# Kernel optimization log

Measured on AMD Instinct MI355X. Metric: run time of the kernel, lower is better.

The kernel has to match this reference:

```python
import jax, jax.numpy as jnp
import numpy as np

ND, NT, B = 16384, 16384, 4096
FD, FT, C = 256, 256, 768


def _gat(x_src, x_dst, ei, Ws, Wd, a_s, a_d, b, num_dst, self_loops):
    """PyG GATConv, heads=1: per-edge attention softmax over incoming edges."""
    if self_loops:
        loops = jnp.arange(num_dst, dtype=ei.dtype)
        ei = jnp.concatenate([ei, jnp.stack([loops, loops])], axis=1)
    src, dst = ei[0], ei[1]
    hs = x_src @ Ws                                   # [Ns, C]
    hd = x_dst @ Wd                                   # [Ndst, C]
    e = jax.nn.leaky_relu((hs @ a_s)[src] + (hd @ a_d)[dst], 0.2)   # [E]
    m = jax.ops.segment_max(e, dst, num_segments=num_dst)
    p = jnp.exp(e - m[dst])
    s = jax.ops.segment_sum(p, dst, num_segments=num_dst)
    alpha = p / (s[dst] + 1e-16)
    out = jax.ops.segment_sum(hs[src] * alpha[:, None], dst, num_segments=num_dst)
    return out + b


def _l2norm(x):
    n = jnp.linalg.norm(x, axis=1, keepdims=True)
    return x / jnp.maximum(n, 1e-12)


def setup_inputs() -> dict:
    ks = iter(jax.random.split(jax.random.key(0), 64))
    def nrm(shape, fan_in=None):
        s = 1.0 if fan_in is None else (1.0 / fan_in) ** 0.5
        return jax.random.normal(next(ks), shape, jnp.float32) * s
    inp = {}
    inp["x_drug"] = nrm((ND, FD))
    inp["x_target"] = nrm((NT, FT))
    inp["cell_features"] = nrm((B, 890))
    for et, fs, fd in (("dd", FD, FD), ("dt", FD, FT), ("tt", FT, FT)):
        inp[f"W_src_{et}"] = nrm((fs, C), fs)
        inp[f"W_dst_{et}"] = nrm((fd, C), fd)
        inp[f"a_src_{et}"] = nrm((C,), C)
        inp[f"a_dst_{et}"] = nrm((C,), C)
        inp[f"b_{et}"] = jnp.zeros((C,), jnp.float32)
    for name, fi, fo in (("red1", 890, 2048), ("red2", 2048, 512), ("red3", 512, 2 * C),
                         ("r2a", 4 * C, 2048), ("r2b", 2048, 512), ("r2c", 512, C), ("cls", C, 2)):
        inp[f"{name}_w"] = nrm((fi, fo), fi)
        inp[f"{name}_b"] = jnp.zeros((fo,), jnp.float32)
    inp["drug1_id"] = jax.random.randint(next(ks), (B,), 0, ND)
    inp["drug2_id"] = jax.random.randint(next(ks), (B,), 0, ND)
    inp["ei_dd"] = jax.random.randint(next(ks), (2, 131072), 0, ND)
    inp["ei_dt"] = jnp.stack([jax.random.randint(next(ks), (262144,), 0, ND),
                              jax.random.randint(next(ks), (262144,), 0, NT)])
    inp["ei_tt"] = jax.random.randint(next(ks), (2, 262144), 0, NT)
    return inp


def reference(x_drug, x_target, cell_features,
              W_src_dd, W_dst_dd, a_src_dd, a_dst_dd, b_dd,
              W_src_dt, W_dst_dt, a_src_dt, a_dst_dt, b_dt,
              W_src_tt, W_dst_tt, a_src_tt, a_dst_tt, b_tt,
              red1_w, red1_b, red2_w, red2_b, red3_w, red3_b,
              r2a_w, r2a_b, r2b_w, r2b_b, r2c_w, r2c_b,
              cls_w, cls_b,
              drug1_id, drug2_id, ei_dd, ei_dt, ei_tt):
    # HeteroConv (aggr='sum') followed by per-type ReLU, num_layers=1
    drug = jax.nn.relu(_gat(x_drug, x_drug, ei_dd,
                            W_src_dd, W_dst_dd, a_src_dd, a_dst_dd, b_dd, ND, True))
    target = jax.nn.relu(
        _gat(x_drug, x_target, ei_dt, W_src_dt, W_dst_dt, a_src_dt, a_dst_dt, b_dt, NT, False)
        + _gat(x_target, x_target, ei_tt, W_src_tt, W_dst_tt, a_src_tt, a_dst_tt, b_tt, NT, True))
    del target  # with num_layers=1 the target embeddings never feed the output (faithful)
    d1 = drug[drug1_id]
    d2 = drug[drug2_id]
    cell = _l2norm(cell_features)
    cell = jax.nn.relu(cell @ red1_w + red1_b)
    cell = jax.nn.relu(cell @ red2_w + red2_b)
    cell = jax.nn.relu(cell @ red3_w + red3_b)          # [B, 2*C]
    hidden = _l2norm(jnp.concatenate([d1, d2, cell], axis=1))  # [B, 4*C]
    hidden = jax.nn.relu(hidden @ r2a_w + r2a_b)
    hidden = jax.nn.relu(hidden @ r2b_w + r2b_b)
    hidden = jax.nn.relu(hidden @ r2c_w + r2c_b)
    return hidden @ cls_w + cls_b                       # [B, 2]
```

## Files before the change

### kernel.cpp

```cpp
#include <hip/hip_runtime.h>
#include <cstdint>

#define ND 16384
#define BATCH 4096
#define CDIM 768
#define E_DD 131072
#define FD 256

typedef unsigned short u16;
typedef u16 u16x4 __attribute__((ext_vector_type(4)));
typedef u16 u16x8 __attribute__((ext_vector_type(8)));
typedef short s16x8 __attribute__((ext_vector_type(8)));
typedef float f32x4 __attribute__((ext_vector_type(4)));

__device__ __forceinline__ u16 f2bf(float x) {
  union { float f; uint32_t u; } v; v.f = x;
  uint32_t r = v.u + 0x7fffu + ((v.u >> 16) & 1u);
  return (u16)(r >> 16);
}
__device__ __forceinline__ float bf2f(u16 h) {
  union { float f; uint32_t u; } v; v.u = ((uint32_t)h) << 16;
  return v.f;
}
__device__ __forceinline__ uint32_t split2p(float x) {
  u16 h = f2bf(x);
  u16 l = f2bf(x - bf2f(h));
  return ((uint32_t)h << 16) | l;
}

#define GLOAD_LDS16(gp, lp)                                                   \
  __builtin_amdgcn_global_load_lds(                                           \
      (__attribute__((address_space(1))) void*)(gp),                          \
      (__attribute__((address_space(3))) void*)(lp), 16, 0, 0)

#define KP 40

template <int KS, int OUT_BF16, int RELU, int BIAS, int ASPLIT, int ALO, int BLO,
          int BKD, int NW>
__device__ __forceinline__ void gemm_core(
    int bx, int by, int bz,
    const float* __restrict__ Af,
    const u16* __restrict__ Ahi, const u16* __restrict__ Alo,
    const u16* __restrict__ Bhi, const u16* __restrict__ Blo,
    const float* __restrict__ bias,
    float* __restrict__ Cf, u16* __restrict__ Chi,
    int M, int N, int K, u16* AsB, u16* BsB) {
  constexpr int NTH = NW * 64;
  constexpr int WC = (NW == 8) ? 4 : 2;
  constexpr int MT = 4;
  constexpr int NT = (NW == 8) ? 2 : 4;
  constexpr int BM = 128, BN = 128;
  constexpr int ASEG = BM / 64;
  constexpr int BSEG = BN / 64;
  constexpr bool DIRECT = (ASPLIT == 0 && ALO == 0 && BLO == 0);

  const int t = threadIdx.x;
  const int bm0 = bx * BM, bn0 = by * BN;
  const int wid = t >> 6, lane = t & 63;
  const int quad = lane >> 4, l16 = lane & 15;
  const int wm0 = (wid / WC) * (MT * 16);
  const int wn0 = (wid % WC) * (NT * 16);

  const int chunk = K / KS;
  const int kbeg = (KS > 1) ? bz * chunk : 0;
  const int kend = kbeg + chunk;

  float bvv[NT];
#pragma unroll
  for (int ni = 0; ni < NT; ++ni)
    bvv[ni] = BIAS ? bias[bn0 + wn0 + ni * 16 + l16] : 0.f;

  f32x4 acc[MT][NT];
#pragma unroll
  for (int i = 0; i < MT; ++i)
#pragma unroll
    for (int j = 0; j < NT; ++j) acc[i][j] = (f32x4){0.f, 0.f, 0.f, 0.f};

  if constexpr (DIRECT) {
    constexpr int SLOTS = BKD / 8;
    constexpr int SM = SLOTS - 1;
    constexpr int NLD = (BM * BKD) / (NTH * 8);
    auto stageA = [&](int buf, int kk) {
#pragma unroll
      for (int c = 0; c < NLD; ++c) {
        int s = t + NTH * c;
        int r = s / SLOTS, j = s % SLOTS;
        int jj = j ^ (r & SM);
        size_t goff = (size_t)(bm0 + r) * K + kk + jj * 8;
        int lofs = __builtin_amdgcn_readfirstlane((wid * 64 + NTH * c) * 8);
        GLOAD_LDS16(Ahi + goff, AsB + buf * (BM * BKD) + lofs);
      }
    };
    auto stageB = [&](int buf, int kk) {
#pragma unroll
      for (int c = 0; c < NLD; ++c) {
        int s = t + NTH * c;
        int r = s / SLOTS, j = s % SLOTS;
        int jj = j ^ (r & SM);
        size_t goff = (size_t)(bn0 + r) * K + kk + jj * 8;
        int lofs = __builtin_amdgcn_readfirstlane((wid * 64 + NTH * c) * 8);
        GLOAD_LDS16(Bhi + goff, BsB + buf * (BN * BKD) + lofs);
      }
    };
    const int rsw = l16 & SM;
    stageA(0, kbeg);
    stageB(0, kbeg);
    int cur = 0;
    for (int k0 = kbeg;;) {
      __syncthreads();
      int kn = k0 + BKD;
      if (kn < kend) {
        stageA(cur ^ 1, kn);
        stageB(cur ^ 1, kn);
      }
      const u16* Ab = AsB + cur * (BM * BKD);
      const u16* Bb = BsB + cur * (BN * BKD);
#pragma unroll
      for (int h = 0; h < BKD / 32; ++h) {
        s16x8 ah[MT], bh[NT];
#pragma unroll
        for (int mi = 0; mi < MT; ++mi)
          ah[mi] = *(const s16x8*)(Ab + (wm0 + mi * 16 + l16) * BKD +
                                   (((h * 4 + quad) ^ rsw) * 8));
#pragma unroll
        for (int ni = 0; ni < NT; ++ni)
          bh[ni] = *(const s16x8*)(Bb + (wn0 + ni * 16 + l16) * BKD +
                                   (((h * 4 + quad) ^ rsw) * 8));
#pragma unroll
        for (int mi = 0; mi < MT; ++mi)
#pragma unroll
          for (int ni = 0; ni < NT; ++ni)
            acc[mi][ni] = __builtin_amdgcn_mfma_f32_16x16x32_bf16(
                ah[mi], bh[ni], acc[mi][ni], 0, 0, 0);
      }
      k0 = kn;
      cur ^= 1;
      if (k0 >= kend) break;
    }
  } else {
    auto As = [&](int a, int r, int k) -> u16& { return AsB[(a * BM + r) * KP + k]; };
    auto Bs = [&](int a, int r, int k) -> u16& { return BsB[(a * BN + r) * KP + k]; };

    u16x8 pAh[ASEG], pAl[ASEG], pBh[BSEG], pBl[BSEG];

    auto loadA = [&](int c, int kk) {
      int s = t + 256 * c, row = s >> 2, kq = (s & 3) * 8;
      size_t off = (size_t)(bm0 + row) * K + kk + kq;
      if (ASPLIT) {
        f32x4 v0 = *(const f32x4*)(Af + off);
        f32x4 v1 = *(const f32x4*)(Af + off + 4);
        u16x8 h, l;
#pragma unroll
        for (int e = 0; e < 4; ++e) {
          uint32_t p = split2p(v0[e]);
          h[e] = (u16)(p >> 16); l[e] = (u16)(p & 0xffffu);
          uint32_t q = split2p(v1[e]);
          h[e + 4] = (u16)(q >> 16); l[e + 4] = (u16)(q & 0xffffu);
        }
        pAh[c] = h; pAl[c] = l;
      } else {
        pAh[c] = *(const u16x8*)(Ahi + off);
        if (ALO) pAl[c] = *(const u16x8*)(Alo + off);
      }
    };
    auto loadB = [&](int c, int kk) {
      int s = t + 256 * c, row = s >> 2, kq = (s & 3) * 8;
      size_t off = (size_t)(bn0 + row) * K + kk + kq;
      pBh[c] = *(const u16x8*)(Bhi + off);
      if (BLO) pBl[c] = *(const u16x8*)(Blo + off);
    };

#pragma unroll
    for (int c = 0; c < ASEG; ++c) loadA(c, kbeg);
#pragma unroll
    for (int c = 0; c < BSEG; ++c) loadB(c, kbeg);

    for (int k0 = kbeg;;) {
      __syncthreads();
#pragma unroll
      for (int c = 0; c < ASEG; ++c) {
        int s = t + 256 * c, row = s >> 2, kq = (s & 3) * 8;
        *(u16x8*)&As(0, row, kq) = pAh[c];
        if (ALO) *(u16x8*)&As(1, row, kq) = pAl[c];
      }
#pragma unroll
      for (int c = 0; c < BSEG; ++c) {
        int s = t + 256 * c, row = s >> 2, kq = (s & 3) * 8;
        *(u16x8*)&Bs(0, row, kq) = pBh[c];
        if (BLO) *(u16x8*)&Bs(1, row, kq) = pBl[c];
      }
      __syncthreads();

      int kn = k0 + 32;
      if (kn < kend) {
#pragma unroll
        for (int c = 0; c < ASEG; ++c) loadA(c, kn);
#pragma unroll
        for (int c = 0; c < BSEG; ++c) loadB(c, kn);
      }

      s16x8 ah[MT], al[MT], bh[NT], bl[NT];
#pragma unroll
      for (int mi = 0; mi < MT; ++mi) {
        ah[mi] = *(const s16x8*)&As(0, wm0 + mi * 16 + l16, quad * 8);
        if (ALO) al[mi] = *(const s16x8*)&As(1, wm0 + mi * 16 + l16, quad * 8);
      }
#pragma unroll
      for (int ni = 0; ni < NT; ++ni) {
        bh[ni] = *(const s16x8*)&Bs(0, wn0 + ni * 16 + l16, quad * 8);
        if (BLO) bl[ni] = *(const s16x8*)&Bs(1, wn0 + ni * 16 + l16, quad * 8);
      }
#pragma unroll
      for (int mi = 0; mi < MT; ++mi)
#pragma unroll
        for (int ni = 0; ni < NT; ++ni) {
          acc[mi][ni] = __builtin_amdgcn_mfma_f32_16x16x32_bf16(
              ah[mi], bh[ni], acc[mi][ni], 0, 0, 0);
          if (BLO)
            acc[mi][ni] = __builtin_amdgcn_mfma_f32_16x16x32_bf16(
                ah[mi], bl[ni], acc[mi][ni], 0, 0, 0);
          if (ALO)
            acc[mi][ni] = __builtin_amdgcn_mfma_f32_16x16x32_bf16(
                al[mi], bh[ni], acc[mi][ni], 0, 0, 0);
        }
      k0 = kn;
      if (k0 >= kend) break;
    }
  }

  float* Cp = (KS > 1) ? Cf + (size_t)bz * M * N : Cf;
#pragma unroll
  for (int mi = 0; mi < MT; ++mi) {
#pragma unroll
    for (int ni = 0; ni < NT; ++ni) {
      int row = bm0 + wm0 + mi * 16 + quad * 4;
      int col = bn0 + wn0 + ni * 16 + l16;
#pragma unroll
      for (int r = 0; r < 4; ++r) {
        float v = acc[mi][ni][r] + bvv[ni];
        if (RELU) v = fmaxf(v, 0.f);
        size_t o = (size_t)(row + r) * N + col;
        if (OUT_BF16) Chi[o] = f2bf(v);
        else Cp[o] = v;
      }
    }
  }
}

template <int KS, int OUT_BF16, int RELU, int BIAS, int ASPLIT, int ALO, int BLO,
          int BKD, int NW>
__global__ __launch_bounds__(NW * 64) void mfma_gemm(
    const float* __restrict__ Af,
    const u16* __restrict__ Ahi, const u16* __restrict__ Alo,
    const u16* __restrict__ Bhi, const u16* __restrict__ Blo,
    const float* __restrict__ bias,
    float* __restrict__ Cf, u16* __restrict__ Chi,
    int M, int N, int K) {
  constexpr bool DIRECT = (ASPLIT == 0 && ALO == 0 && BLO == 0);
  __shared__ __align__(16) u16 AsB[DIRECT ? 2 * 128 * BKD : (ALO ? 2 : 1) * 128 * KP];
  __shared__ __align__(16) u16 BsB[DIRECT ? 2 * 128 * BKD : (BLO ? 2 : 1) * 128 * KP];
  gemm_core<KS, OUT_BF16, RELU, BIAS, ASPLIT, ALO, BLO, BKD, NW>(
      blockIdx.x, blockIdx.y, (KS > 1) ? (int)blockIdx.z : 0,
      Af, Ahi, Alo, Bhi, Blo, bias, Cf, Chi, M, N, K, AsB, BsB);
}

__device__ __forceinline__ void gat_body(
    int idx, int t,
    const u16* __restrict__ hs, const float* __restrict__ es,
    const float* __restrict__ ed, const int* __restrict__ offsets,
    const int* __restrict__ slots, const float* __restrict__ bias,
    const int* __restrict__ list, const int* __restrict__ cnt,
    u16* __restrict__ out) {
  if (idx >= *cnt) return;
  int d = list[idx];
  int lane = t & 63;
  int beg = offsets[d], end = offsets[d + 1];
  float edv = ed[d];
  float mx = -1e30f;
  for (int j = beg + lane; j < end; j += 64) {
    float e = es[slots[j]] + edv;
    e = e >= 0.f ? e : 0.2f * e;
    mx = fmaxf(mx, e);
  }
#pragma unroll
  for (int m = 32; m; m >>= 1) mx = fmaxf(mx, __shfl_xor(mx, m));
  float sm = 0.f;
  for (int j = beg + lane; j < end; j += 64) {
    float e = es[slots[j]] + edv;
    e = e >= 0.f ? e : 0.2f * e;
    sm += expf(e - mx);
  }
#pragma unroll
  for (int m = 32; m; m >>= 1) sm += __shfl_xor(sm, m);
  float inv = 1.f / (sm + 1e-16f);
  int c8 = lane * 8;
  int c4 = 512 + lane * 4;
  float a8[8] = {};
  float a4[4] = {};
  for (int j = beg; j < end; ++j) {
    int srcn = slots[j];
    float e = es[srcn] + edv;
    e = e >= 0.f ? e : 0.2f * e;
    float alpha = expf(e - mx) * inv;
    const u16* hrow = hs + (size_t)srcn * CDIM;
    u16x8 r8 = *(const u16x8*)(hrow + c8);
    u16x4 r4 = *(const u16x4*)(hrow + c4);
#pragma unroll
    for (int e2 = 0; e2 < 8; ++e2) a8[e2] = fmaf(alpha, bf2f(r8[e2]), a8[e2]);
#pragma unroll
    for (int e2 = 0; e2 < 4; ++e2) a4[e2] = fmaf(alpha, bf2f(r4[e2]), a4[e2]);
  }
  u16* orow = out + (size_t)d * CDIM;
  u16x8 o8;
  u16x4 o4;
#pragma unroll
  for (int e2 = 0; e2 < 8; ++e2) o8[e2] = f2bf(fmaxf(a8[e2] + bias[c8 + e2], 0.f));
#pragma unroll
  for (int e2 = 0; e2 < 4; ++e2) o4[e2] = f2bf(fmaxf(a4[e2] + bias[c4 + e2], 0.f));
  *(u16x8*)(orow + c8) = o8;
  *(u16x4*)(orow + c4) = o4;
}

__global__ __launch_bounds__(256) void gat_aggregate(
    const u16* __restrict__ hs, const float* __restrict__ es,
    const float* __restrict__ ed, const int* __restrict__ offsets,
    const int* __restrict__ slots, const float* __restrict__ bias,
    const int* __restrict__ list, const int* __restrict__ cnt,
    u16* __restrict__ out) {
  gat_body(blockIdx.x * 4 + (threadIdx.x >> 6), threadIdx.x,
           hs, es, ed, offsets, slots, bias, list, cnt, out);
}

__global__ __launch_bounds__(256) void dual_gemm_red1_hs_scatter(
    const u16* __restrict__ cn, const u16* __restrict__ r1T,
    const float* __restrict__ red1_b, u16* __restrict__ c1,
    const float* __restrict__ xd, const u16* __restrict__ wsrcT,
    u16* __restrict__ hs,
    const int* __restrict__ src, const int* __restrict__ dst,
    int* __restrict__ cursor, int* __restrict__ slots) {
  __shared__ __align__(16) u16 SMEM[16384];
  int b = blockIdx.x;
  if (b < 512) {
    gemm_core<1, 1, 1, 1, 0, 0, 0, 32, 4>(b & 31, b >> 5, 0, nullptr, cn, nullptr,
                                          r1T, nullptr, red1_b, nullptr, c1,
                                          BATCH, 2048, 896, SMEM, SMEM + 2 * 128 * 32);
  } else if (b < 1280) {
    int b2 = b - 512;
    gemm_core<1, 1, 0, 0, 1, 1, 0, 32, 4>(b2 & 127, b2 >> 7, 0, xd, nullptr, nullptr,
                                          wsrcT, nullptr, nullptr, nullptr, hs,
                                          ND, CDIM, FD, SMEM, SMEM + 2 * 128 * KP);
  } else {
    int e = (b - 1280) * 256 + threadIdx.x;
    if (e < E_DD) {
      int pos = atomicAdd(&cursor[dst[e]], 1);
      slots[pos] = src[e];
    }
  }
}

template <int KS>
__global__ void reduce_split_ks(const float* __restrict__ P,
                                const float* __restrict__ bias,
                                u16* __restrict__ Chi, int M, int N) {
  int i = blockIdx.x * 256 + threadIdx.x;
  int total = (M * N) >> 2;
  if (i >= total) return;
  f32x4 s = ((const f32x4*)P)[i];
#pragma unroll
  for (int z = 1; z < KS; ++z) s += ((const f32x4*)P)[(size_t)z * total + i];
  int col = (i * 4) % N;
  f32x4 bv = *(const f32x4*)(bias + col);
  u16x4 h;
#pragma unroll
  for (int e = 0; e < 4; ++e) h[e] = f2bf(fmaxf(s[e] + bv[e], 0.f));
  *(u16x4*)&Chi[i * 4] = h;
}

__global__ void reduce_cls(const float* __restrict__ P,
                           const float* __restrict__ bias,
                           const float* __restrict__ clsw,
                           const float* __restrict__ clsb,
                           float* __restrict__ out) {
  int row = blockIdx.x * 4 + (threadIdx.x >> 6);
  int lane = threadIdx.x & 63;
  const f32x4* p0 = (const f32x4*)(P + (size_t)row * CDIM);
  const f32x4* p1 = (const f32x4*)(P + (size_t)BATCH * CDIM + (size_t)row * CDIM);
  float s0 = 0.f, s1 = 0.f;
#pragma unroll
  for (int i = 0; i < 3; ++i) {
    int c4 = lane + 64 * i;
    f32x4 a = p0[c4] + p1[c4];
    f32x4 bv = *(const f32x4*)(bias + c4 * 4);
#pragma unroll
    for (int e = 0; e < 4; ++e) {
      float h = fmaxf(a[e] + bv[e], 0.f);
      int c = c4 * 4 + e;
      s0 = fmaf(h, clsw[c * 2 + 0], s0);
      s1 = fmaf(h, clsw[c * 2 + 1], s1);
    }
  }
#pragma unroll
  for (int m = 32; m; m >>= 1) {
    s0 += __shfl_xor(s0, m);
    s1 += __shfl_xor(s1, m);
  }
  if (lane == 0) {
    out[row * 2 + 0] = s0 + clsb[0];
    out[row * 2 + 1] = s1 + clsb[1];
  }
}

struct TDesc {
  const float* W;
  u16* Th;
  int K, N, Kpad, start;
};
struct TPack { TDesc d[7]; };

#define P1_T 11328
#define P1_W (P1_T + 256)
#define P1_I (P1_W + 64)
__global__ __launch_bounds__(256) void prep1(
    TPack p,
    const float* __restrict__ Wsrc, const float* __restrict__ Wdst,
    const float* __restrict__ a_s, const float* __restrict__ a_d,
    float* __restrict__ wsv, float* __restrict__ wdv,
    int* __restrict__ counts, int* __restrict__ mask, int* __restrict__ cnt,
    const float* __restrict__ cellf, u16* __restrict__ cn_hi) {
  __shared__ __align__(16) float S[1088];
  int b = blockIdx.x;
  int t = threadIdx.x;
  if (b < P1_T) {
    float (*tile)[33] = (float(*)[33])S;
    int mi = 0;
#pragma unroll
    for (int i = 1; i < 7; ++i)
      if (b >= p.d[i].start) mi = i;
    TDesc dd = p.d[mi];
    int rel = b - dd.start;
    int tilesX = dd.Kpad / 32;
    int k0 = (rel % tilesX) * 32, n0 = (rel / tilesX) * 32;
    int tx = t & 31, ty = t >> 5;
#pragma unroll
    for (int i = 0; i < 4; ++i) {
      int k = k0 + ty + 8 * i, n = n0 + tx;
      tile[ty + 8 * i][tx] = (k < dd.K && n < dd.N) ? dd.W[(size_t)k * dd.N + n] : 0.f;
    }
    __syncthreads();
#pragma unroll
    for (int i = 0; i < 4; ++i) {
      int n = n0 + ty + 8 * i, k = k0 + tx;
      if (n < dd.N) dd.Th[(size_t)n * dd.Kpad + k] = f2bf(tile[tx][ty + 8 * i]);
    }
  } else if (b < P1_W) {
    int k = b - P1_T;
    float* rs = S;
    float* rd = S + 256;
    float s = 0.f, d = 0.f;
    for (int c = t; c < CDIM; c += 256) {
      s += Wsrc[(size_t)k * CDIM + c] * a_s[c];
      d += Wdst[(size_t)k * CDIM + c] * a_d[c];
    }
    rs[t] = s; rd[t] = d;
    __syncthreads();
    for (int st = 128; st; st >>= 1) {
      if (t < st) { rs[t] += rs[t + st]; rd[t] += rd[t + st]; }
      __syncthreads();
    }
    if (t == 0) { wsv[k] = rs[0]; wdv[k] = rd[0]; }
  } else if (b < P1_I) {
    int i = (b - P1_W) * 256 + t;
    if (i < ND) { counts[i] = 1; mask[i] = 0; }
    if (i == 0) *cnt = 0;
  } else {
    int row = b - P1_I;
    float* red = S;
    const float* irow = cellf + (size_t)row * 890;
    float s = 0.f;
    for (int c = t; c < 890; c += 256) { float v = irow[c]; s += v * v; }
    red[t] = s;
    __syncthreads();
    for (int st = 128; st; st >>= 1) {
      if (t < st) red[t] += red[t + st];
      __syncthreads();
    }
    float inv = 1.f / fmaxf(sqrtf(red[0]), 1e-12f);
    for (int c = t; c < 896; c += 256) {
      float v = (c < 890) ? irow[c] * inv : 0.f;
      cn_hi[(size_t)row * 896 + c] = f2bf(v);
    }
  }
}

#define P2_E (ND * FD / 1024)
#define P2_M (P2_E + BATCH / 256)
__global__ __launch_bounds__(256) void prep2(
    const float* __restrict__ x, const float* __restrict__ wsv,
    const float* __restrict__ wdv, float* __restrict__ es, float* __restrict__ ed,
    const int* __restrict__ d1, const int* __restrict__ d2, int* __restrict__ mask,
    const int* __restrict__ dst, int* __restrict__ counts) {
  int b = blockIdx.x, t = threadIdx.x;
  if (b < P2_E) {
    int i = b * 256 + t;
    int lane = t & 63;
    int row = i >> 6;
    int c4 = lane * 4;
    f32x4 v = ((const f32x4*)x)[i];
    f32x4 ws = *(const f32x4*)(wsv + c4);
    f32x4 wd = *(const f32x4*)(wdv + c4);
    float a = v[0] * ws[0] + v[1] * ws[1] + v[2] * ws[2] + v[3] * ws[3];
    float bb = v[0] * wd[0] + v[1] * wd[1] + v[2] * wd[2] + v[3] * wd[3];
#pragma unroll
    for (int m = 32; m; m >>= 1) {
      a += __shfl_xor(a, m);
      bb += __shfl_xor(bb, m);
    }
    if (lane == 0) { es[row] = a; ed[row] = bb; }
  } else if (b < P2_M) {
    int i = (b - P2_E) * 256 + t;
    mask[d1[i]] = 1;
    mask[d2[i]] = 1;
  } else {
    int e = (b - P2_M) * 256 + t;
    atomicAdd(&counts[dst[e]], 1);
  }
}

__global__ __launch_bounds__(512) void prep3(
    const int* __restrict__ mask, int* __restrict__ cnt, int* __restrict__ list,
    const int* __restrict__ counts, int* __restrict__ offsets,
    int* __restrict__ cursor, int* __restrict__ slots) {
  __shared__ int part[512];
  int b = blockIdx.x, t = threadIdx.x;
  if (b < 32) {
    int i = b * 512 + t;
    if (mask[i]) {
      int pos = atomicAdd(cnt, 1);
      list[pos] = i;
    }
  } else {
    int base = t * 32;
    int s = 0;
    for (int i = 0; i < 32; ++i) s += counts[base + i];
    part[t] = s;
    __syncthreads();
    if (t == 0) {
      int run = 0;
      for (int i = 0; i < 512; ++i) { int tmp = part[i]; part[i] = run; run += tmp; }
      offsets[ND] = run;
    }
    __syncthreads();
    int run = part[t];
    for (int i = 0; i < 32; ++i) {
      int d = base + i;
      offsets[d] = run;
      slots[run] = d;
      cursor[d] = run + 1;
      run += counts[d];
    }
  }
}

__global__ __launch_bounds__(256) void hidden_build_bf16(
    const u16* __restrict__ drug, const u16* __restrict__ c3,
    const int* __restrict__ d1, const int* __restrict__ d2,
    u16* __restrict__ hhi) {
  int row = blockIdx.x;
  int t = threadIdx.x;
  const u16* s1 = drug + (size_t)d1[row] * CDIM;
  const u16* s2 = drug + (size_t)d2[row] * CDIM;
  const u16* s3 = c3 + (size_t)row * (2 * CDIM);
  float vals[12];
  float ss = 0.f;
#pragma unroll
  for (int i = 0; i < 12; ++i) {
    int c = t + 256 * i;
    float v;
    if (i < 3)      v = bf2f(s1[c]);
    else if (i < 6) v = bf2f(s2[c - CDIM]);
    else            v = bf2f(s3[c - 2 * CDIM]);
    vals[i] = v;
    ss += v * v;
  }
  __shared__ float red[256];
  red[t] = ss;
  __syncthreads();
  for (int st = 128; st; st >>= 1) {
    if (t < st) red[t] += red[t + st];
    __syncthreads();
  }
  float inv = 1.f / fmaxf(sqrtf(red[0]), 1e-12f);
  u16* hrow_h = hhi + (size_t)row * (4 * CDIM);
#pragma unroll
  for (int i = 0; i < 12; ++i) hrow_h[t + 256 * i] = f2bf(vals[i] * inv);
}

extern "C" void kernel_launch(void* const* d_in, const int* in_sizes, int n_in,
                              void* d_out, int out_size, void* d_ws, size_t ws_size,
                              hipStream_t stream) {
  const float* x_drug   = (const float*)d_in[0];
  const float* cellf    = (const float*)d_in[2];
  const float* W_src_dd = (const float*)d_in[3];
  const float* W_dst_dd = (const float*)d_in[4];
  const float* a_src_dd = (const float*)d_in[5];
  const float* a_dst_dd = (const float*)d_in[6];
  const float* b_dd     = (const float*)d_in[7];
  const float* red1_w = (const float*)d_in[18];
  const float* red1_b = (const float*)d_in[19];
  const float* red2_w = (const float*)d_in[20];
  const float* red2_b = (const float*)d_in[21];
  const float* red3_w = (const float*)d_in[22];
  const float* red3_b = (const float*)d_in[23];
  const float* r2a_w  = (const float*)d_in[24];
  const float* r2a_b  = (const float*)d_in[25];
  const float* r2b_w  = (const float*)d_in[26];
  const float* r2b_b  = (const float*)d_in[27];
  const float* r2c_w  = (const float*)d_in[28];
  const float* r2c_b  = (const float*)d_in[29];
  const float* cls_w  = (const float*)d_in[30];
  const float* cls_b  = (const float*)d_in[31];
  const int* drug1_id = (const int*)d_in[32];
  const int* drug2_id = (const int*)d_in[33];
  const int* ei_dd    = (const int*)d_in[34];
  float* out = (float*)d_out;

  const int* dd_src = ei_dd;
  const int* dd_dst = ei_dd + E_DD;

  char* w = (char*)d_ws;
  size_t off = 0;
  auto alloc = [&](size_t bytes) -> char* {
    char* p = w + off;
    off = (off + bytes + 255) & ~(size_t)255;
    return p;
  };
  u16* hs   = (u16*)alloc((size_t)ND * CDIM * 2);
  u16* drug = (u16*)alloc((size_t)ND * CDIM * 2);
  u16* c3   = (u16*)alloc((size_t)BATCH * 2 * CDIM * 2);
  float* P  = (float*)alloc((size_t)4 * BATCH * 512 * 4);
  u16* hid_hi = hs;
  u16* cn_hi = (u16*)alloc((size_t)BATCH * 896 * 2);
  u16* c1_hi = (u16*)alloc((size_t)BATCH * 2048 * 2);
  u16* c2_hi = (u16*)alloc((size_t)BATCH * 512 * 2);
  u16* wsrcT_hi = (u16*)alloc((size_t)CDIM * FD * 2);
  u16* r1T_hi = (u16*)alloc((size_t)2048 * 896 * 2);
  u16* r2T_hi = (u16*)alloc((size_t)512 * 2048 * 2);
  u16* r3T_hi = (u16*)alloc((size_t)1536 * 512 * 2);
  u16* raT_hi = (u16*)alloc((size_t)2048 * 3072 * 2);
  u16* rbT_hi = (u16*)alloc((size_t)512 * 2048 * 2);
  u16* rcT_hi = (u16*)alloc((size_t)768 * 512 * 2);
  float* es  = (float*)alloc((size_t)ND * 4);
  float* ed  = (float*)alloc((size_t)ND * 4);
  float* wsv = (float*)alloc(FD * 4);
  float* wdv = (float*)alloc(FD * 4);
  int* counts  = (int*)alloc((size_t)ND * 4);
  int* offsets = (int*)alloc((size_t)(ND + 1) * 4);
  int* cursor  = (int*)alloc((size_t)ND * 4);
  int* slots   = (int*)alloc((size_t)(E_DD + ND) * 4);
  int* mask    = (int*)alloc((size_t)ND * 4);
  int* list    = (int*)alloc((size_t)ND * 4);
  int* cnt     = (int*)alloc(256);
  (void)ws_size; (void)n_in; (void)in_sizes; (void)out_size;

  TPack tp;
  tp.d[0] = {W_src_dd, wsrcT_hi, 256, 768, 256, 0};
  tp.d[1] = {red1_w, r1T_hi, 890, 2048, 896, 192};
  tp.d[2] = {red2_w, r2T_hi, 2048, 512, 2048, 1984};
  tp.d[3] = {red3_w, r3T_hi, 512, 1536, 512, 3008};
  tp.d[4] = {r2a_w, raT_hi, 3072, 2048, 3072, 3776};
  tp.d[5] = {r2b_w, rbT_hi, 2048, 512, 2048, 9920};
  tp.d[6] = {r2c_w, rcT_hi, 512, 768, 512, 10944};
  prep1<<<15744, 256, 0, stream>>>(tp, W_src_dd, W_dst_dd, a_src_dd, a_dst_dd,
                                   wsv, wdv, counts, mask, cnt, cellf, cn_hi);

  prep2<<<4624, 256, 0, stream>>>(x_drug, wsv, wdv, es, ed, drug1_id, drug2_id,
                                  mask, dd_dst, counts);

  prep3<<<33, 512, 0, stream>>>(mask, cnt, list, counts, offsets, cursor, slots);

  dual_gemm_red1_hs_scatter<<<1792, 256, 0, stream>>>(
      cn_hi, r1T_hi, red1_b, c1_hi, x_drug, wsrcT_hi, hs,
      dd_src, dd_dst, cursor, slots);

  mfma_gemm<4, 0, 0, 0, 0, 0, 0, 64, 8><<<dim3(BATCH / 128, 512 / 128, 4), 512, 0, stream>>>(
      nullptr, c1_hi, nullptr, r2T_hi, nullptr, nullptr, P, nullptr, BATCH, 512, 2048);
  reduce_split_ks<4><<<BATCH * 512 / 1024, 256, 0, stream>>>(P, red2_b, c2_hi, BATCH, 512);
  mfma_gemm<1, 1, 1, 1, 0, 0, 0, 64, 8><<<dim3(BATCH / 128, 1536 / 128), 512, 0, stream>>>(
      nullptr, c2_hi, nullptr, r3T_hi, nullptr, red3_b, nullptr, c3, BATCH, 1536, 512);

  gat_aggregate<<<ND / 4, 256, 0, stream>>>(hs, es, ed, offsets, slots, b_dd, list, cnt, drug);

  hidden_build_bf16<<<BATCH, 256, 0, stream>>>(drug, c3, drug1_id, drug2_id, hid_hi);

  mfma_gemm<1, 1, 1, 1, 0, 0, 0, 64, 8><<<dim3(BATCH / 128, 2048 / 128), 512, 0, stream>>>(
      nullptr, hid_hi, nullptr, raT_hi, nullptr, r2a_b, nullptr, c1_hi, BATCH, 2048, 3072);
  mfma_gemm<4, 0, 0, 0, 0, 0, 0, 64, 8><<<dim3(BATCH / 128, 512 / 128, 4), 512, 0, stream>>>(
      nullptr, c1_hi, nullptr, rbT_hi, nullptr, nullptr, P, nullptr, BATCH, 512, 2048);
  reduce_split_ks<4><<<BATCH * 512 / 1024, 256, 0, stream>>>(P, r2b_b, c2_hi, BATCH, 512);
  mfma_gemm<2, 0, 0, 0, 0, 0, 0, 64, 8><<<dim3(BATCH / 128, CDIM / 128, 2), 512, 0, stream>>>(
      nullptr, c2_hi, nullptr, rcT_hi, nullptr, nullptr, P, nullptr, BATCH, CDIM, 512);
  reduce_cls<<<BATCH / 4, 256, 0, stream>>>(P, r2c_b, cls_w, cls_b, out);
}
```

Measured before the change: 441.5 us.

## Pre-split x_drug into concatenated hi/lo bf16 and run hs GEMM on direct-LDS path

The hs projection previously split fp32 x_drug into hi/lo bf16 inside the GEMM and used a register-staged path with two MFMAs per tile. Now prep2 writes x_drug as [hi|lo] bf16 along K (512 wide) and the W_src transpose is duplicated along K, so hi*W + lo*W becomes one K=512 GEMM on the async global_load_lds double-buffered path. This removes the slower non-direct GEMM branch entirely. In exchange it adds an extra 16 MB write in prep2 and extra reads in the GEMM.

New measurement: 433.6 us. About the same (-1.8%).

```diff
diff --git a/kernel.cpp b/kernel.cpp
--- a/kernel.cpp
+++ b/kernel.cpp
@@ -22,11 +22,6 @@
   union { float f; uint32_t u; } v; v.u = ((uint32_t)h) << 16;
   return v.f;
 }
-__device__ __forceinline__ uint32_t split2p(float x) {
-  u16 h = f2bf(x);
-  u16 l = f2bf(x - bf2f(h));
-  return ((uint32_t)h << 16) | l;
-}
 
 #define GLOAD_LDS16(gp, lp)                                                   \
   __builtin_amdgcn_global_load_lds(                                           \
@@ -35,13 +30,10 @@
 
 #define KP 40
 
-template <int KS, int OUT_BF16, int RELU, int BIAS, int ASPLIT, int ALO, int BLO,
-          int BKD, int NW>
+template <int KS, int OUT_BF16, int RELU, int BIAS, int BKD, int NW>
 __device__ __forceinline__ void gemm_core(
     int bx, int by, int bz,
-    const float* __restrict__ Af,
-    const u16* __restrict__ Ahi, const u16* __restrict__ Alo,
-    const u16* __restrict__ Bhi, const u16* __restrict__ Blo,
+    const u16* __restrict__ Ahi, const u16* __restrict__ Bhi,
     const float* __restrict__ bias,
     float* __restrict__ Cf, u16* __restrict__ Chi,
     int M, int N, int K, u16* AsB, u16* BsB) {
@@ -50,9 +42,6 @@
   constexpr int MT = 4;
   constexpr int NT = (NW == 8) ? 2 : 4;
   constexpr int BM = 128, BN = 128;
-  constexpr int ASEG = BM / 64;
-  constexpr int BSEG = BN / 64;
-  constexpr bool DIRECT = (ASPLIT == 0 && ALO == 0 && BLO == 0);
 
   const int t = threadIdx.x;
   const int bm0 = bx * BM, bn0 = by * BN;
@@ -76,156 +65,65 @@
 #pragma unroll
     for (int j = 0; j < NT; ++j) acc[i][j] = (f32x4){0.f, 0.f, 0.f, 0.f};
 
-  if constexpr (DIRECT) {
-    constexpr int SLOTS = BKD / 8;
-    constexpr int SM = SLOTS - 1;
-    constexpr int NLD = (BM * BKD) / (NTH * 8);
-    auto stageA = [&](int buf, int kk) {
-#pragma unroll
-      for (int c = 0; c < NLD; ++c) {
-        int s = t + NTH * c;
-        int r = s / SLOTS, j = s % SLOTS;
-        int jj = j ^ (r & SM);
-        size_t goff = (size_t)(bm0 + r) * K + kk + jj * 8;
-        int lofs = __builtin_amdgcn_readfirstlane((wid * 64 + NTH * c) * 8);
-        GLOAD_LDS16(Ahi + goff, AsB + buf * (BM * BKD) + lofs);
-      }
-    };
-    auto stageB = [&](int buf, int kk) {
-#pragma unroll
-      for (int c = 0; c < NLD; ++c) {
-        int s = t + NTH * c;
-        int r = s / SLOTS, j = s % SLOTS;
-        int jj = j ^ (r & SM);
-        size_t goff = (size_t)(bn0 + r) * K + kk + jj * 8;
-        int lofs = __builtin_amdgcn_readfirstlane((wid * 64 + NTH * c) * 8);
-        GLOAD_LDS16(Bhi + goff, BsB + buf * (BN * BKD) + lofs);
-      }
-    };
-    const int rsw = l16 & SM;
-    stageA(0, kbeg);
-    stageB(0, kbeg);
-    int cur = 0;
-    for (int k0 = kbeg;;) {
-      __syncthreads();
-      int kn = k0 + BKD;
-      if (kn < kend) {
-        stageA(cur ^ 1, kn);
-        stageB(cur ^ 1, kn);
-      }
-      const u16* Ab = AsB + cur * (BM * BKD);
-      const u16* Bb = BsB + cur * (BN * BKD);
-#pragma unroll
-      for (int h = 0; h < BKD / 32; ++h) {
-        s16x8 ah[MT], bh[NT];
-#pragma unroll
-        for (int mi = 0; mi < MT; ++mi)
-          ah[mi] = *(const s16x8*)(Ab + (wm0 + mi * 16 + l16) * BKD +
-                                   (((h * 4 + quad) ^ rsw) * 8));
+  constexpr int SLOTS = BKD / 8;
+  constexpr int SM = SLOTS - 1;
+  constexpr int NLD = (BM * BKD) / (NTH * 8);
+  auto stageA = [&](int buf, int kk) {
+#pragma unroll
+    for (int c = 0; c < NLD; ++c) {
+      int s = t + NTH * c;
+      int r = s / SLOTS, j = s % SLOTS;
+      int jj = j ^ (r & SM);
+      size_t goff = (size_t)(bm0 + r) * K + kk + jj * 8;
+      int lofs = __builtin_amdgcn_readfirstlane((wid * 64 + NTH * c) * 8);
+      GLOAD_LDS16(Ahi + goff, AsB + buf * (BM * BKD) + lofs);
+    }
+  };
+  auto stageB = [&](int buf, int kk) {
+#pragma unroll
+    for (int c = 0; c < NLD; ++c) {
+      int s = t + NTH * c;
+      int r = s / SLOTS, j = s % SLOTS;
+      int jj = j ^ (r & SM);
+      size_t goff = (size_t)(bn0 + r) * K + kk + jj * 8;
+      int lofs = __builtin_amdgcn_readfirstlane((wid * 64 + NTH * c) * 8);
+      GLOAD_LDS16(Bhi + goff, BsB + buf * (BN * BKD) + lofs);
+    }
+  };
+  const int rsw = l16 & SM;
+  stageA(0, kbeg);
+  stageB(0, kbeg);
+  int cur = 0;
+  for (int k0 = kbeg;;) {
+    __syncthreads();
+    int kn = k0 + BKD;
+    if (kn < kend) {
+      stageA(cur ^ 1, kn);
+      stageB(cur ^ 1, kn);
+    }
+    const u16* Ab = AsB + cur * (BM * BKD);
+    const u16* Bb = BsB + cur * (BN * BKD);
+#pragma unroll
+    for (int h = 0; h < BKD / 32; ++h) {
+      s16x8 ah[MT], bh[NT];
+#pragma unroll
+      for (int mi = 0; mi < MT; ++mi)
+        ah[mi] = *(const s16x8*)(Ab + (wm0 + mi * 16 + l16) * BKD +
+                                 (((h * 4 + quad) ^ rsw) * 8));
+#pragma unroll
+      for (int ni = 0; ni < NT; ++ni)
+        bh[ni] = *(const s16x8*)(Bb + (wn0 + ni * 16 + l16) * BKD +
+                                 (((h * 4 + quad) ^ rsw) * 8));
+#pragma unroll
+      for (int mi = 0; mi < MT; ++mi)
 #pragma unroll
         for (int ni = 0; ni < NT; ++ni)
-          bh[ni] = *(const s16x8*)(Bb + (wn0 + ni * 16 + l16) * BKD +
-                                   (((h * 4 + quad) ^ rsw) * 8));
-#pragma unroll
-        for (int mi = 0; mi < MT; ++mi)
-#pragma unroll
-          for (int ni = 0; ni < NT; ++ni)
-            acc[mi][ni] = __builtin_amdgcn_mfma_f32_16x16x32_bf16(
-                ah[mi], bh[ni], acc[mi][ni], 0, 0, 0);
-      }
-      k0 = kn;
-      cur ^= 1;
-      if (k0 >= kend) break;
-    }
-  } else {
-    auto As = [&](int a, int r, int k) -> u16& { return AsB[(a * BM + r) * KP + k]; };
-    auto Bs = [&](int a, int r, int k) -> u16& { return BsB[(a * BN + r) * KP + k]; };
-
-    u16x8 pAh[ASEG], pAl[ASEG], pBh[BSEG], pBl[BSEG];
-
-    auto loadA = [&](int c, int kk) {
-      int s = t + 256 * c, row = s >> 2, kq = (s & 3) * 8;
-      size_t off = (size_t)(bm0 + row) * K + kk + kq;
-      if (ASPLIT) {
-        f32x4 v0 = *(const f32x4*)(Af + off);
-        f32x4 v1 = *(const f32x4*)(Af + off + 4);
-        u16x8 h, l;
-#pragma unroll
-        for (int e = 0; e < 4; ++e) {
-          uint32_t p = split2p(v0[e]);
-          h[e] = (u16)(p >> 16); l[e] = (u16)(p & 0xffffu);
-          uint32_t q = split2p(v1[e]);
-          h[e + 4] = (u16)(q >> 16); l[e + 4] = (u16)(q & 0xffffu);
-        }
-        pAh[c] = h; pAl[c] = l;
-      } else {
-        pAh[c] = *(const u16x8*)(Ahi + off);
-        if (ALO) pAl[c] = *(const u16x8*)(Alo + off);
-      }
-    };
-    auto loadB = [&](int c, int kk) {
-      int s = t + 256 * c, row = s >> 2, kq = (s & 3) * 8;
-      size_t off = (size_t)(bn0 + row) * K + kk + kq;
-      pBh[c] = *(const u16x8*)(Bhi + off);
-      if (BLO) pBl[c] = *(const u16x8*)(Blo + off);
-    };
-
-#pragma unroll
-    for (int c = 0; c < ASEG; ++c) loadA(c, kbeg);
-#pragma unroll
-    for (int c = 0; c < BSEG; ++c) loadB(c, kbeg);
-
-    for (int k0 = kbeg;;) {
-      __syncthreads();
-#pragma unroll
-      for (int c = 0; c < ASEG; ++c) {
-        int s = t + 256 * c, row = s >> 2, kq = (s & 3) * 8;
-        *(u16x8*)&As(0, row, kq) = pAh[c];
-        if (ALO) *(u16x8*)&As(1, row, kq) = pAl[c];
-      }
-#pragma unroll
-      for (int c = 0; c < BSEG; ++c) {
-        int s = t + 256 * c, row = s >> 2, kq = (s & 3) * 8;
-        *(u16x8*)&Bs(0, row, kq) = pBh[c];
-        if (BLO) *(u16x8*)&Bs(1, row, kq) = pBl[c];
-      }
-      __syncthreads();
-
-      int kn = k0 + 32;
-      if (kn < kend) {
-#pragma unroll
-        for (int c = 0; c < ASEG; ++c) loadA(c, kn);
-#pragma unroll
-        for (int c = 0; c < BSEG; ++c) loadB(c, kn);
-      }
-
-      s16x8 ah[MT], al[MT], bh[NT], bl[NT];
-#pragma unroll
-      for (int mi = 0; mi < MT; ++mi) {
-        ah[mi] = *(const s16x8*)&As(0, wm0 + mi * 16 + l16, quad * 8);
-        if (ALO) al[mi] = *(const s16x8*)&As(1, wm0 + mi * 16 + l16, quad * 8);
-      }
-#pragma unroll
-      for (int ni = 0; ni < NT; ++ni) {
-        bh[ni] = *(const s16x8*)&Bs(0, wn0 + ni * 16 + l16, quad * 8);
-        if (BLO) bl[ni] = *(const s16x8*)&Bs(1, wn0 + ni * 16 + l16, quad * 8);
-      }
-#pragma unroll
-      for (int mi = 0; mi < MT; ++mi)
-#pragma unroll
-        for (int ni = 0; ni < NT; ++ni) {
           acc[mi][ni] = __builtin_amdgcn_mfma_f32_16x16x32_bf16(
               ah[mi], bh[ni], acc[mi][ni], 0, 0, 0);
-          if (BLO)
-            acc[mi][ni] = __builtin_amdgcn_mfma_f32_16x16x32_bf16(
-                ah[mi], bl[ni], acc[mi][ni], 0, 0, 0);
-          if (ALO)
-            acc[mi][ni] = __builtin_amdgcn_mfma_f32_16x16x32_bf16(
-                al[mi], bh[ni], acc[mi][ni], 0, 0, 0);
-        }
-      k0 = kn;
-      if (k0 >= kend) break;
-    }
+    }
+    k0 = kn;
+    cur ^= 1;
+    if (k0 >= kend) break;
   }
 
   float* Cp = (KS > 1) ? Cf + (size_t)bz * M * N : Cf;
@@ -247,21 +145,17 @@
   }
 }
 
-template <int KS, int OUT_BF16, int RELU, int BIAS, int ASPLIT, int ALO, int BLO,
-          int BKD, int NW>
+template <int KS, int OUT_BF16, int RELU, int BIAS, int BKD, int NW>
 __global__ __launch_bounds__(NW * 64) void mfma_gemm(
-    const float* __restrict__ Af,
-    const u16* __restrict__ Ahi, const u16* __restrict__ Alo,
-    const u16* __restrict__ Bhi, const u16* __restrict__ Blo,
+    const u16* __restrict__ Ahi, const u16* __restrict__ Bhi,
     const float* __restrict__ bias,
     float* __restrict__ Cf, u16* __restrict__ Chi,
     int M, int N, int K) {
-  constexpr bool DIRECT = (ASPLIT == 0 && ALO == 0 && BLO == 0);
-  __shared__ __align__(16) u16 AsB[DIRECT ? 2 * 128 * BKD : (ALO ? 2 : 1) * 128 * KP];
-  __shared__ __align__(16) u16 BsB[DIRECT ? 2 * 128 * BKD : (BLO ? 2 : 1) * 128 * KP];
-  gemm_core<KS, OUT_BF16, RELU, BIAS, ASPLIT, ALO, BLO, BKD, NW>(
+  __shared__ __align__(16) u16 AsB[2 * 128 * BKD];
+  __shared__ __align__(16) u16 BsB[2 * 128 * BKD];
+  gemm_core<KS, OUT_BF16, RELU, BIAS, BKD, NW>(
       blockIdx.x, blockIdx.y, (KS > 1) ? (int)blockIdx.z : 0,
-      Af, Ahi, Alo, Bhi, Blo, bias, Cf, Chi, M, N, K, AsB, BsB);
+      Ahi, Bhi, bias, Cf, Chi, M, N, K, AsB, BsB);
 }
 
 __device__ __forceinline__ void gat_body(
@@ -334,21 +228,21 @@
 __global__ __launch_bounds__(256) void dual_gemm_red1_hs_scatter(
     const u16* __restrict__ cn, const u16* __restrict__ r1T,
     const float* __restrict__ red1_b, u16* __restrict__ c1,
-    const float* __restrict__ xd, const u16* __restrict__ wsrcT,
+    const u16* __restrict__ x2, const u16* __restrict__ wsrcT2,
     u16* __restrict__ hs,
     const int* __restrict__ src, const int* __restrict__ dst,
     int* __restrict__ cursor, int* __restrict__ slots) {
   __shared__ __align__(16) u16 SMEM[16384];
   int b = blockIdx.x;
   if (b < 512) {
-    gemm_core<1, 1, 1, 1, 0, 0, 0, 32, 4>(b & 31, b >> 5, 0, nullptr, cn, nullptr,
-                                          r1T, nullptr, red1_b, nullptr, c1,
-                                          BATCH, 2048, 896, SMEM, SMEM + 2 * 128 * 32);
+    gemm_core<1, 1, 1, 1, 32, 4>(b & 31, b >> 5, 0, cn, r1T, red1_b,
+                                 nullptr, c1, BATCH, 2048, 896,
+                                 SMEM, SMEM + 2 * 128 * 32);
   } else if (b < 1280) {
     int b2 = b - 512;
-    gemm_core<1, 1, 0, 0, 1, 1, 0, 32, 4>(b2 & 127, b2 >> 7, 0, xd, nullptr, nullptr,
-                                          wsrcT, nullptr, nullptr, nullptr, hs,
-                                          ND, CDIM, FD, SMEM, SMEM + 2 * 128 * KP);
+    gemm_core<1, 1, 0, 0, 32, 4>(b2 & 127, b2 >> 7, 0, x2, wsrcT2, nullptr,
+                                 nullptr, hs, ND, CDIM, 512,
+                                 SMEM, SMEM + 2 * 128 * 32);
   } else {
     int e = (b - 1280) * 256 + threadIdx.x;
     if (e < E_DD) {
@@ -413,7 +307,7 @@
 struct TDesc {
   const float* W;
   u16* Th;
-  int K, N, Kpad, start;
+  int K, N, Kpad, start, dup;
 };
 struct TPack { TDesc d[7]; };
 
@@ -438,7 +332,7 @@
       if (b >= p.d[i].start) mi = i;
     TDesc dd = p.d[mi];
     int rel = b - dd.start;
-    int tilesX = dd.Kpad / 32;
+    int tilesX = dd.dup ? (dd.K / 32) : (dd.Kpad / 32);
     int k0 = (rel % tilesX) * 32, n0 = (rel / tilesX) * 32;
     int tx = t & 31, ty = t >> 5;
 #pragma unroll
@@ -450,7 +344,11 @@
 #pragma unroll
     for (int i = 0; i < 4; ++i) {
       int n = n0 + ty + 8 * i, k = k0 + tx;
-      if (n < dd.N) dd.Th[(size_t)n * dd.Kpad + k] = f2bf(tile[tx][ty + 8 * i]);
+      if (n < dd.N) {
+        u16 v = f2bf(tile[tx][ty + 8 * i]);
+        dd.Th[(size_t)n * dd.Kpad + k] = v;
+        if (dd.dup) dd.Th[(size_t)n * dd.Kpad + k + dd.K] = v;
+      }
     }
   } else if (b < P1_W) {
     int k = b - P1_T;
@@ -497,6 +395,7 @@
 __global__ __launch_bounds__(256) void prep2(
     const float* __restrict__ x, const float* __restrict__ wsv,
     const float* __restrict__ wdv, float* __restrict__ es, float* __restrict__ ed,
+    u16* __restrict__ x2,
     const int* __restrict__ d1, const int* __restrict__ d2, int* __restrict__ mask,
     const int* __restrict__ dst, int* __restrict__ counts) {
   int b = blockIdx.x, t = threadIdx.x;
@@ -510,6 +409,15 @@
     f32x4 wd = *(const f32x4*)(wdv + c4);
     float a = v[0] * ws[0] + v[1] * ws[1] + v[2] * ws[2] + v[3] * ws[3];
     float bb = v[0] * wd[0] + v[1] * wd[1] + v[2] * wd[2] + v[3] * wd[3];
+    u16x4 hi, lo;
+#pragma unroll
+    for (int e = 0; e < 4; ++e) {
+      u16 h = f2bf(v[e]);
+      hi[e] = h;
+      lo[e] = f2bf(v[e] - bf2f(h));
+    }
+    *(u16x4*)(x2 + (size_t)row * 512 + c4) = hi;
+    *(u16x4*)(x2 + (size_t)row * 512 + 256 + c4) = lo;
 #pragma unroll
     for (int m = 32; m; m >>= 1) {
       a += __shfl_xor(a, m);
@@ -642,7 +550,8 @@
   u16* cn_hi = (u16*)alloc((size_t)BATCH * 896 * 2);
   u16* c1_hi = (u16*)alloc((size_t)BATCH * 2048 * 2);
   u16* c2_hi = (u16*)alloc((size_t)BATCH * 512 * 2);
-  u16* wsrcT_hi = (u16*)alloc((size_t)CDIM * FD * 2);
+  u16* x2 = (u16*)alloc((size_t)ND * 512 * 2);
+  u16* wsrcT2 = (u16*)alloc((size_t)CDIM * 512 * 2);
   u16* r1T_hi = (u16*)alloc((size_t)2048 * 896 * 2);
   u16* r2T_hi = (u16*)alloc((size_t)512 * 2048 * 2);
   u16* r3T_hi = (u16*)alloc((size_t)1536 * 512 * 2);
@@ -663,41 +572,41 @@
   (void)ws_size; (void)n_in; (void)in_sizes; (void)out_size;
 
   TPack tp;
-  tp.d[0] = {W_src_dd, wsrcT_hi, 256, 768, 256, 0};
-  tp.d[1] = {red1_w, r1T_hi, 890, 2048, 896, 192};
-  tp.d[2] = {red2_w, r2T_hi, 2048, 512, 2048, 1984};
-  tp.d[3] = {red3_w, r3T_hi, 512, 1536, 512, 3008};
-  tp.d[4] = {r2a_w, raT_hi, 3072, 2048, 3072, 3776};
-  tp.d[5] = {r2b_w, rbT_hi, 2048, 512, 2048, 9920};
-  tp.d[6] = {r2c_w, rcT_hi, 512, 768, 512, 10944};
+  tp.d[0] = {W_src_dd, wsrcT2, 256, 768, 512, 0, 1};
+  tp.d[1] = {red1_w, r1T_hi, 890, 2048, 896, 192, 0};
+  tp.d[2] = {red2_w, r2T_hi, 2048, 512, 2048, 1984, 0};
+  tp.d[3] = {red3_w, r3T_hi, 512, 1536, 512, 3008, 0};
+  tp.d[4] = {r2a_w, raT_hi, 3072, 2048, 3072, 3776, 0};
+  tp.d[5] = {r2b_w, rbT_hi, 2048, 512, 2048, 9920, 0};
+  tp.d[6] = {r2c_w, rcT_hi, 512, 768, 512, 10944, 0};
   prep1<<<15744, 256, 0, stream>>>(tp, W_src_dd, W_dst_dd, a_src_dd, a_dst_dd,
                                    wsv, wdv, counts, mask, cnt, cellf, cn_hi);
 
-  prep2<<<4624, 256, 0, stream>>>(x_drug, wsv, wdv, es, ed, drug1_id, drug2_id,
-                                  mask, dd_dst, counts);
+  prep2<<<4624, 256, 0, stream>>>(x_drug, wsv, wdv, es, ed, x2, drug1_id,
+                                  drug2_id, mask, dd_dst, counts);
 
   prep3<<<33, 512, 0, stream>>>(mask, cnt, list, counts, offsets, cursor, slots);
 
   dual_gemm_red1_hs_scatter<<<1792, 256, 0, stream>>>(
-      cn_hi, r1T_hi, red1_b, c1_hi, x_drug, wsrcT_hi, hs,
+      cn_hi, r1T_hi, red1_b, c1_hi, x2, wsrcT2, hs,
       dd_src, dd_dst, cursor, slots);
 
-  mfma_gemm<4, 0, 0, 0, 0, 0, 0, 64, 8><<<dim3(BATCH / 128, 512 / 128, 4), 512, 0, stream>>>(
-      nullptr, c1_hi, nullptr, r2T_hi, nullptr, nullptr, P, nullptr, BATCH, 512, 2048);
+  mfma_gemm<4, 0, 0, 0, 64, 8><<<dim3(BATCH / 128, 512 / 128, 4), 512, 0, stream>>>(
+      c1_hi, r2T_hi, nullptr, P, nullptr, BATCH, 512, 2048);
   reduce_split_ks<4><<<BATCH * 512 / 1024, 256, 0, stream>>>(P, red2_b, c2_hi, BATCH, 512);
-  mfma_gemm<1, 1, 1, 1, 0, 0, 0, 64, 8><<<dim3(BATCH / 128, 1536 / 128), 512, 0, stream>>>(
-      nullptr, c2_hi, nullptr, r3T_hi, nullptr, red3_b, nullptr, c3, BATCH, 1536, 512);
+  mfma_gemm<1, 1, 1, 1, 64, 8><<<dim3(BATCH / 128, 1536 / 128), 512, 0, stream>>>(
+      c2_hi, r3T_hi, red3_b, nullptr, c3, BATCH, 1536, 512);
 
   gat_aggregate<<<ND / 4, 256, 0, stream>>>(hs, es, ed, offsets, slots, b_dd, list, cnt, drug);
 
   hidden_build_bf16<<<BATCH, 256, 0, stream>>>(drug, c3, drug1_id, drug2_id, hid_hi);
 
-  mfma_gemm<1, 1, 1, 1, 0, 0, 0, 64, 8><<<dim3(BATCH / 128, 2048 / 128), 512, 0, stream>>>(
-      nullptr, hid_hi, nullptr, raT_hi, nullptr, r2a_b, nullptr, c1_hi, BATCH, 2048, 3072);
-  mfma_gemm<4, 0, 0, 0, 0, 0, 0, 64, 8><<<dim3(BATCH / 128, 512 / 128, 4), 512, 0, stream>>>(
-      nullptr, c1_hi, nullptr, rbT_hi, nullptr, nullptr, P, nullptr, BATCH, 512, 2048);
+  mfma_gemm<1, 1, 1, 1, 64, 8><<<dim3(BATCH / 128, 2048 / 128), 512, 0, stream>>>(
+      hid_hi, raT_hi, r2a_b, nullptr, c1_hi, BATCH, 2048, 3072);
+  mfma_gemm<4, 0, 0, 0, 64, 8><<<dim3(BATCH / 128, 512 / 128, 4), 512, 0, stream>>>(
+      c1_hi, rbT_hi, nullptr, P, nullptr, BATCH, 512, 2048);
   reduce_split_ks<4><<<BATCH * 512 / 1024, 256, 0, stream>>>(P, r2b_b, c2_hi, BATCH, 512);
-  mfma_gemm<2, 0, 0, 0, 0, 0, 0, 64, 8><<<dim3(BATCH / 128, CDIM / 128, 2), 512, 0, stream>>>(
-      nullptr, c2_hi, nullptr, rcT_hi, nullptr, nullptr, P, nullptr, BATCH, CDIM, 512);
+  mfma_gemm<2, 0, 0, 0, 64, 8><<<dim3(BATCH / 128, CDIM / 128, 2), 512, 0, stream>>>(
+      c2_hi, rcT_hi, nullptr, P, nullptr, BATCH, CDIM, 512);
   reduce_cls<<<BATCH / 4, 256, 0, stream>>>(P, r2c_b, cls_w, cls_b, out);
 }
```
